# Optimization experiments

Hardware: AMD Instinct MI355X
Metric: run time of the kernel (lower is better)

## Reference

```python
import jax, jax.numpy as jnp
import numpy as np

N_NODES = 50000


def _gcn_norm(edge_index, n):
    # Add self-loops (PyG GCNConv default) and compute symmetric normalization.
    src = jnp.concatenate([edge_index[0], jnp.arange(n, dtype=edge_index.dtype)])
    dst = jnp.concatenate([edge_index[1], jnp.arange(n, dtype=edge_index.dtype)])
    deg = jax.ops.segment_sum(jnp.ones(src.shape[0], dtype=jnp.float32), dst,
                              num_segments=n)
    dinv = jnp.where(deg > 0, jax.lax.rsqrt(deg), 0.0)
    norm = dinv[src] * dinv[dst]  # [E+N]
    return src, dst, norm


def _gcn_conv(x, src, dst, norm, W, b, n):
    h = x @ W                              # [N, out] linear transform first
    msgs = h[src] * norm[:, None]          # gather + edge-wise scale [E+N, out]
    out = jax.ops.segment_sum(msgs, dst, num_segments=n)  # scatter-add
    return out + b


def setup_inputs() -> dict:
    key = jax.random.key(0)
    k1, k2, k3, k4 = jax.random.split(key, 4)
    N, E, F, H, C = N_NODES, 1600000, 128, 128, 64
    x = jax.random.normal(k1, (N, F), dtype=jnp.float32)
    edge_index = jax.random.randint(k2, (2, E), 0, N, dtype=jnp.int64)
    W1 = jax.random.normal(k3, (F, H), dtype=jnp.float32) * 0.05
    b1 = jnp.zeros((H,), dtype=jnp.float32)
    W2 = jax.random.normal(k4, (H, C), dtype=jnp.float32) * 0.05
    b2 = jnp.zeros((C,), dtype=jnp.float32)
    return {"x": x, "edge_index": edge_index, "W1": W1, "b1": b1,
            "W2": W2, "b2": b2}


def reference(x, edge_index, W1, b1, W2, b2):
    n = x.shape[0]
    src, dst, norm = _gcn_norm(edge_index, n)
    h = _gcn_conv(x, src, dst, norm, W1, b1, n)
    h = jax.nn.relu(h)
    out = _gcn_conv(h, src, dst, norm, W2, b2, n)
    return out
```

## Files before the change

### kernel.cpp

```cpp
#include <hip/hip_runtime.h>
#include <hip/hip_bf16.h>
#include <stdint.h>

#define N_NODES 50000
#define N_EDGES 1600000
#define N_TOT   (N_EDGES + N_NODES)
#define NBKT      256
#define BKT_NODES 196
#define BKT_CAP   7168
#define TILE      4096
#define EPT       16
#define ZROW      N_NODES

typedef unsigned short u16;
typedef __attribute__((ext_vector_type(8))) short short8;
typedef __attribute__((ext_vector_type(4))) float floatx4;

__device__ __forceinline__ float b2f(u16 u) {
    union { unsigned int i; float f; } v; v.i = ((unsigned int)u) << 16; return v.f;
}
__device__ __forceinline__ float asf(unsigned u) {
    union { unsigned int i; float f; } v; v.i = u; return v.f;
}
__device__ __forceinline__ u16 f2b(float f) {
    union { unsigned int i; float f; } v; v.f = f;
    unsigned int r = (v.i + 0x7FFFu + ((v.i >> 16) & 1u)) >> 16;
    return (u16)r;
}

__global__ __launch_bounds__(256) void k_part(const int* __restrict__ ei,
                                              const unsigned* __restrict__ xw,
                                              int* __restrict__ flags,
                                              unsigned* __restrict__ pairs,
                                              int* __restrict__ bktcnt) {
    __shared__ unsigned pairsL[TILE];
    __shared__ unsigned char bktL[TILE];
    __shared__ int hist[NBKT], incl[NBKT], delta[NBKT];
    __shared__ int zc, pc;
    int tid = threadIdx.x;
    long base = (long)blockIdx.x * TILE;
    hist[tid] = 0;
    if (tid == 0) { zc = 0; pc = 0; }
    __syncthreads();
    unsigned hw = ((const unsigned*)ei)[2 * tid + 1];
    atomicAdd(&zc, hw == 0 ? 1 : 0);
    if (blockIdx.x == 0) {
        unsigned w = xw[tid];
        int ex = (w >> 7) & 0xFF;
        atomicAdd(&pc, ((ex == 0) || (ex >= 0x60 && ex <= 0x9F)) ? 1 : 0);
    }
    __syncthreads();
    int i64 = zc > 250;
    if (blockIdx.x == 0 && tid == 0) {
        flags[0] = (pc < 160) ? 1 : 0;
        flags[1] = i64;
    }

    int myb[EPT], myrank[EPT]; unsigned myp[EPT];
#pragma unroll
    for (int t = 0; t < EPT; t++) {
        long idx = base + t * 256 + tid;
        int b = -1; unsigned p = 0;
        if (idx < N_TOT) {
            int s, d;
            if (idx < N_EDGES) {
                if (i64) { s = ei[2 * idx]; d = ei[2 * (N_EDGES + idx)]; }
                else     { s = ei[idx];     d = ei[N_EDGES + idx]; }
            } else {
                s = d = (int)(idx - N_EDGES);
            }
            b = d / BKT_NODES;
            p = (unsigned)s | ((unsigned)(d - b * BKT_NODES) << 16);
        }
        myb[t] = b; myp[t] = p;
        myrank[t] = (b >= 0) ? atomicAdd(&hist[b], 1) : 0;
    }
    __syncthreads();

    int tot = hist[tid];
    incl[tid] = tot;
    __syncthreads();
    for (int o = 1; o < NBKT; o <<= 1) {
        int t2 = (tid >= o) ? incl[tid - o] : 0;
        __syncthreads();
        incl[tid] += t2;
        __syncthreads();
    }
    int excl = incl[tid] - tot;
    int gb = atomicAdd(&bktcnt[tid], tot);
    hist[tid]  = excl;
    delta[tid] = tid * BKT_CAP + gb - excl;
    __syncthreads();

#pragma unroll
    for (int t = 0; t < EPT; t++) {
        if (myb[t] >= 0) {
            int slot = hist[myb[t]] + myrank[t];
            pairsL[slot] = myp[t];
            bktL[slot]   = (unsigned char)myb[t];
        }
    }
    __syncthreads();
    int count = incl[NBKT - 1];
    for (int i = tid; i < count; i += 256) {
        int b = bktL[i];
        int pos = delta[b] + i;
        if (pos - b * BKT_CAP < BKT_CAP)
            pairs[pos] = pairsL[i];
    }
}

__global__ __launch_bounds__(256) void k_bucket(const unsigned* __restrict__ pairs,
                                                const int* __restrict__ bktcnt,
                                                int* __restrict__ rowstart,
                                                int* __restrict__ deg,
                                                float* __restrict__ dinv,
                                                u16* __restrict__ csr) {
    __shared__ u16 csrL[BKT_CAP];
    __shared__ int degL[NBKT], curL[NBKT], scanT[NBKT];
    int b = blockIdx.x, tid = threadIdx.x;
    int cv = bktcnt[tid];
    scanT[tid] = cv;
    __syncthreads();
    for (int o = 1; o < NBKT; o <<= 1) {
        int t = (tid >= o) ? scanT[tid - o] : 0;
        __syncthreads();
        scanT[tid] += t;
        __syncthreads();
    }
    int cnt  = bktcnt[b];
    int base = scanT[b] - cnt;
    __syncthreads();

    const unsigned* reg = pairs + (size_t)b * BKT_CAP;
    degL[tid] = 0;
    __syncthreads();
    for (int i = tid; i < cnt; i += 256)
        atomicAdd(&degL[reg[i] >> 16], 1);
    __syncthreads();
    int v = degL[tid];
    scanT[tid] = v;
    __syncthreads();
    for (int o = 1; o < NBKT; o <<= 1) {
        int t = (tid >= o) ? scanT[tid - o] : 0;
        __syncthreads();
        scanT[tid] += t;
        __syncthreads();
    }
    int excl = scanT[tid] - v;
    curL[tid] = excl;
    int n = b * BKT_NODES + tid;
    if (tid < BKT_NODES && n < N_NODES) {
        rowstart[n] = base + excl;
        deg[n]      = v;
        dinv[n]     = rsqrtf((float)v);
    }
    __syncthreads();
    for (int i = tid; i < cnt; i += 256) {
        unsigned p = reg[i];
        int slot = atomicAdd(&curL[p >> 16], 1);
        csrL[slot] = (u16)(p & 0xFFFFu);
    }
    __syncthreads();
    for (int i = tid; i < cnt; i += 256)
        csr[base + i] = csrL[i];
}

template<int NOUT, bool ADYN>
__global__ __launch_bounds__(256) void k_gemm(const void* __restrict__ A,
                                              const void* __restrict__ W,
                                              const float* __restrict__ dinv,
                                              u16* __restrict__ out, int M,
                                              const int* __restrict__ flags) {
    const int isf32 = flags[0];
    constexpr int LDW = 136;
    __shared__ __align__(16) u16 Wt[NOUT * LDW];
    int tid = threadIdx.x;
    if (blockIdx.x == 0 && tid < NOUT)
        out[(size_t)M * NOUT + tid] = 0;
    const float* Wf = (const float*)W;
    const u16*   Wu = (const u16*)W;
    for (int idx = tid; idx < 128 * NOUT; idx += 256) {
        int k = idx / NOUT, n = idx % NOUT;
        Wt[n * LDW + k] = isf32 ? f2b(Wf[idx]) : Wu[idx];
    }
    __syncthreads();

    int wave = tid >> 6, lane = tid & 63;
    int quad = lane >> 4, l16 = lane & 15;
    int r0 = blockIdx.x * 64 + wave * 16;
    int r = r0 + l16; if (r >= M) r = M - 1;

    floatx4 acc[NOUT / 16];
#pragma unroll
    for (int i = 0; i < NOUT / 16; i++) acc[i] = (floatx4)(0.f);

#pragma unroll
    for (int ks = 0; ks < 4; ks++) {
        short8 a;
        if (ADYN && isf32) {
            const float* af = (const float*)A + (size_t)r * 128 + ks * 32 + quad * 8;
            float4 v0 = ((const float4*)af)[0];
            float4 v1 = ((const float4*)af)[1];
            a[0] = (short)f2b(v0.x); a[1] = (short)f2b(v0.y);
            a[2] = (short)f2b(v0.z); a[3] = (short)f2b(v0.w);
            a[4] = (short)f2b(v1.x); a[5] = (short)f2b(v1.y);
            a[6] = (short)f2b(v1.z); a[7] = (short)f2b(v1.w);
        } else {
            a = ((const short8*)((const u16*)A + (size_t)r * 128))[ks * 4 + quad];
        }
#pragma unroll
        for (int nt = 0; nt < NOUT / 16; nt++) {
            const short8* bp = (const short8*)&Wt[(nt * 16 + l16) * LDW + ks * 32 + quad * 8];
            acc[nt] = __builtin_amdgcn_mfma_f32_16x16x32_bf16(a, *bp, acc[nt], 0, 0, 0);
        }
    }
    float sc[4];
#pragma unroll
    for (int j = 0; j < 4; j++) {
        int row = r0 + quad * 4 + j;
        sc[j] = dinv[row < M ? row : 0];
    }
#pragma unroll
    for (int nt = 0; nt < NOUT / 16; nt++) {
#pragma unroll
        for (int j = 0; j < 4; j++) {
            int row = r0 + quad * 4 + j;
            if (row < M)
                out[(size_t)row * NOUT + nt * 16 + l16] = f2b(acc[nt][j] * sc[j]);
        }
    }
}

#define ACCU(u, j) { acc[j].x += asf((u) << 16); acc[j].y += asf((u) & 0xFFFF0000u); }
#define ACC4(q)    { ACCU(q.x,0) ACCU(q.y,1) ACCU(q.z,2) ACCU(q.w,3) }

__global__ __launch_bounds__(256) void k_agg1(const u16* __restrict__ h,
                                              const u16* __restrict__ csr,
                                              const int* __restrict__ rowstart,
                                              const int* __restrict__ deg,
                                              const float* __restrict__ dinv,
                                              const void* __restrict__ bias,
                                              u16* __restrict__ out,
                                              const int* __restrict__ flags) {
    int wave = threadIdx.x >> 6, lane = threadIdx.x & 63;
    int d = blockIdx.x * 4 + wave;
    int grp = lane >> 4, l16 = lane & 15;
    int start = rowstart[d], dg = deg[d], end = start + dg;
    int rounds = (dg + 3) >> 2;
    const uint4* hb = (const uint4*)h;
    float2 acc[4];
#pragma unroll
    for (int j = 0; j < 4; j++) acc[j] = make_float2(0.f, 0.f);

    int e0 = start + grp;
    int s;
    uint4 q0, q1, q2, q3;
    s = (e0      < end) ? csr[e0]      : ZROW; q0 = hb[(size_t)s * 16 + l16];
    s = (e0 + 4  < end) ? csr[e0 + 4]  : ZROW; q1 = hb[(size_t)s * 16 + l16];
    s = (e0 + 8  < end) ? csr[e0 + 8]  : ZROW; q2 = hb[(size_t)s * 16 + l16];
    s = (e0 + 12 < end) ? csr[e0 + 12] : ZROW; q3 = hb[(size_t)s * 16 + l16];
    int r = 4;
    for (; r + 3 < rounds; r += 4) {
        int e = e0 + 4 * r;
        ACC4(q0) s = (e      < end) ? csr[e]      : ZROW; q0 = hb[(size_t)s * 16 + l16];
        ACC4(q1) s = (e + 4  < end) ? csr[e + 4]  : ZROW; q1 = hb[(size_t)s * 16 + l16];
        ACC4(q2) s = (e + 8  < end) ? csr[e + 8]  : ZROW; q2 = hb[(size_t)s * 16 + l16];
        ACC4(q3) s = (e + 12 < end) ? csr[e + 12] : ZROW; q3 = hb[(size_t)s * 16 + l16];
    }
    for (; r < rounds; r++) {
        int e = e0 + 4 * r;
        ACC4(q0) s = (e < end) ? csr[e] : ZROW;
        q0 = q1; q1 = q2; q2 = q3; q3 = hb[(size_t)s * 16 + l16];
    }
    ACC4(q0) ACC4(q1) ACC4(q2) ACC4(q3)
#pragma unroll
    for (int j = 0; j < 4; j++) {
        acc[j].x += __shfl_xor(acc[j].x, 16); acc[j].y += __shfl_xor(acc[j].y, 16);
        acc[j].x += __shfl_xor(acc[j].x, 32); acc[j].y += __shfl_xor(acc[j].y, 32);
    }
    if (grp == 0) {
        int isf32 = flags[0];
        float dd = dinv[d];
        u16 r8[8];
#pragma unroll
        for (int j = 0; j < 4; j++) {
            float bx = isf32 ? ((const float*)bias)[l16 * 8 + 2 * j]
                             : b2f(((const u16*)bias)[l16 * 8 + 2 * j]);
            float by = isf32 ? ((const float*)bias)[l16 * 8 + 2 * j + 1]
                             : b2f(((const u16*)bias)[l16 * 8 + 2 * j + 1]);
            float vx = acc[j].x * dd + bx;
            float vy = acc[j].y * dd + by;
            r8[2 * j]     = f2b(vx > 0.f ? vx : 0.f);
            r8[2 * j + 1] = f2b(vy > 0.f ? vy : 0.f);
        }
        uint4 o;
        o.x = r8[0] | ((unsigned)r8[1] << 16); o.y = r8[2] | ((unsigned)r8[3] << 16);
        o.z = r8[4] | ((unsigned)r8[5] << 16); o.w = r8[6] | ((unsigned)r8[7] << 16);
        ((uint4*)(out + (size_t)d * 128))[l16] = o;
    }
}

__global__ __launch_bounds__(256) void k_agg2(const u16* __restrict__ h,
                                              const u16* __restrict__ csr,
                                              const int* __restrict__ rowstart,
                                              const int* __restrict__ deg,
                                              const float* __restrict__ dinv,
                                              const void* __restrict__ bias,
                                              float* __restrict__ out,
                                              const int* __restrict__ flags) {
    int wave = threadIdx.x >> 6, lane = threadIdx.x & 63;
    int d = blockIdx.x * 4 + wave;
    int oct = lane >> 3, l8 = lane & 7;
    int start = rowstart[d], dg = deg[d], end = start + dg;
    int rounds = (dg + 7) >> 3;
    const uint4* hb = (const uint4*)h;
    float2 acc[4];
#pragma unroll
    for (int j = 0; j < 4; j++) acc[j] = make_float2(0.f, 0.f);

    int e0 = start + oct;
    int s;
    uint4 q0, q1, q2;
    s = (e0      < end) ? csr[e0]      : ZROW; q0 = hb[(size_t)s * 8 + l8];
    s = (e0 + 8  < end) ? csr[e0 + 8]  : ZROW; q1 = hb[(size_t)s * 8 + l8];
    s = (e0 + 16 < end) ? csr[e0 + 16] : ZROW; q2 = hb[(size_t)s * 8 + l8];
    int r = 3;
    for (; r + 2 < rounds; r += 3) {
        int e = e0 + 8 * r;
        ACC4(q0) s = (e      < end) ? csr[e]      : ZROW; q0 = hb[(size_t)s * 8 + l8];
        ACC4(q1) s = (e + 8  < end) ? csr[e + 8]  : ZROW; q1 = hb[(size_t)s * 8 + l8];
        ACC4(q2) s = (e + 16 < end) ? csr[e + 16] : ZROW; q2 = hb[(size_t)s * 8 + l8];
    }
    for (; r < rounds; r++) {
        int e = e0 + 8 * r;
        ACC4(q0) s = (e < end) ? csr[e] : ZROW;
        q0 = q1; q1 = q2; q2 = hb[(size_t)s * 8 + l8];
    }
    ACC4(q0) ACC4(q1) ACC4(q2)
#pragma unroll
    for (int j = 0; j < 4; j++) {
        acc[j].x += __shfl_xor(acc[j].x, 8);  acc[j].y += __shfl_xor(acc[j].y, 8);
        acc[j].x += __shfl_xor(acc[j].x, 16); acc[j].y += __shfl_xor(acc[j].y, 16);
        acc[j].x += __shfl_xor(acc[j].x, 32); acc[j].y += __shfl_xor(acc[j].y, 32);
    }
    if (oct == 0) {
        int isf32 = flags[0];
        float dd = dinv[d];
        float r8[8];
#pragma unroll
        for (int j = 0; j < 4; j++) {
            float bx = isf32 ? ((const float*)bias)[l8 * 8 + 2 * j]
                             : b2f(((const u16*)bias)[l8 * 8 + 2 * j]);
            float by = isf32 ? ((const float*)bias)[l8 * 8 + 2 * j + 1]
                             : b2f(((const u16*)bias)[l8 * 8 + 2 * j + 1]);
            r8[2 * j]     = acc[j].x * dd + bx;
            r8[2 * j + 1] = acc[j].y * dd + by;
        }
        float4* op = (float4*)(out + (size_t)d * 64) + l8 * 2;
        op[0] = make_float4(r8[0], r8[1], r8[2], r8[3]);
        op[1] = make_float4(r8[4], r8[5], r8[6], r8[7]);
    }
}

extern "C" void kernel_launch(void* const* d_in, const int* in_sizes, int n_in,
                              void* d_out, int out_size, void* d_ws, size_t ws_size,
                              hipStream_t stream) {
    const void* x  = d_in[0];
    const int*  ei = (const int*)d_in[1];
    const void* W1 = d_in[2];
    const void* b1 = d_in[3];
    const void* W2 = d_in[4];
    const void* b2 = d_in[5];
    float* out = (float*)d_out;

    char* ws = (char*)d_ws;
    int*      flags    = (int*)(ws + 0);
    int*      bktcnt   = (int*)(ws + 1024);
    int*      deg      = (int*)(ws + 4096);
    int*      rowstart = (int*)(ws + 204800);
    float*    dinv     = (float*)(ws + 405504);
    unsigned* pairs    = (unsigned*)(ws + 606208);
    u16*      csr      = (u16*)(ws + 7946240);
    u16*      h1       = (u16*)(ws + 11247616);
    u16*      out1     = (u16*)(ws + 24048640);
    u16*      h2       = (u16*)(ws + 606208);

    hipMemsetAsync(bktcnt, 0, NBKT * sizeof(int), stream);
    k_part   <<<(N_TOT + TILE - 1) / TILE, 256, 0, stream>>>(ei, (const unsigned*)x,
                                                             flags, pairs, bktcnt);
    k_bucket <<<NBKT, 256, 0, stream>>>(pairs, bktcnt, rowstart, deg, dinv, csr);

    k_gemm<128, true> <<<(N_NODES + 63) / 64, 256, 0, stream>>>(x, W1, dinv, h1, N_NODES, flags);
    k_agg1<<<N_NODES / 4, 256, 0, stream>>>(h1, csr, rowstart, deg, dinv, b1, out1, flags);
    k_gemm<64, false> <<<(N_NODES + 63) / 64, 256, 0, stream>>>(out1, W2, dinv, h2, N_NODES, flags);
    k_agg2<<<N_NODES / 4, 256, 0, stream>>>(h2, csr, rowstart, deg, dinv, b2, out, flags);
}
```

Before: 246.7 us.

## Split layer-1 features into two 64-column panels for cache-friendly aggregation

The first GEMM now writes h1 as two column panels of 64 features, each with its own zero row. The first aggregation launches twice as many blocks, and each block processes one panel with the 8-lanes-per-edge scheme used by agg2. The goal is to halve the gathered working set per pass so the randomly indexed rows fit better in L2/MALL. In exchange, the CSR indices, rowstart and degree data are read twice, and every node is launched twice.

```diff
diff --git a/kernel.cpp b/kernel.cpp
--- a/kernel.cpp
+++ b/kernel.cpp
@@ -11,6 +11,8 @@
 #define TILE      4096
 #define EPT       16
 #define ZROW      N_NODES
+#define NGRP      12500
+#define PR        (N_NODES + 1)
 
 typedef unsigned short u16;
 typedef __attribute__((ext_vector_type(8))) short short8;
@@ -166,7 +168,7 @@
         csr[base + i] = csrL[i];
 }
 
-template<int NOUT, bool ADYN>
+template<int NOUT, bool ADYN, bool PANEL>
 __global__ __launch_bounds__(256) void k_gemm(const void* __restrict__ A,
                                               const void* __restrict__ W,
                                               const float* __restrict__ dinv,
@@ -176,8 +178,12 @@
     constexpr int LDW = 136;
     __shared__ __align__(16) u16 Wt[NOUT * LDW];
     int tid = threadIdx.x;
-    if (blockIdx.x == 0 && tid < NOUT)
-        out[(size_t)M * NOUT + tid] = 0;
+    if (blockIdx.x == 0 && tid < NOUT) {
+        if (PANEL)
+            out[((size_t)(tid >> 6) * PR + ZROW) * 64 + (tid & 63)] = 0;
+        else
+            out[(size_t)M * NOUT + tid] = 0;
+    }
     const float* Wf = (const float*)W;
     const u16*   Wu = (const u16*)W;
     for (int idx = tid; idx < 128 * NOUT; idx += 256) {
@@ -223,11 +229,17 @@
     }
 #pragma unroll
     for (int nt = 0; nt < NOUT / 16; nt++) {
+        int col = nt * 16 + l16;
 #pragma unroll
         for (int j = 0; j < 4; j++) {
             int row = r0 + quad * 4 + j;
-            if (row < M)
-                out[(size_t)row * NOUT + nt * 16 + l16] = f2b(acc[nt][j] * sc[j]);
+            if (row < M) {
+                u16 val = f2b(acc[nt][j] * sc[j]);
+                if (PANEL)
+                    out[((size_t)(col >> 6) * PR + row) * 64 + (col & 63)] = val;
+                else
+                    out[(size_t)row * NOUT + col] = val;
+            }
         }
     }
 }
@@ -244,51 +256,52 @@
                                               u16* __restrict__ out,
                                               const int* __restrict__ flags) {
     int wave = threadIdx.x >> 6, lane = threadIdx.x & 63;
-    int d = blockIdx.x * 4 + wave;
-    int grp = lane >> 4, l16 = lane & 15;
+    int panel = blockIdx.x / NGRP, gb = blockIdx.x % NGRP;
+    int d = gb * 4 + wave;
+    int oct = lane >> 3, l8 = lane & 7;
     int start = rowstart[d], dg = deg[d], end = start + dg;
-    int rounds = (dg + 3) >> 2;
-    const uint4* hb = (const uint4*)h;
+    int rounds = (dg + 7) >> 3;
+    const uint4* hb = (const uint4*)(h + (size_t)panel * PR * 64);
     float2 acc[4];
 #pragma unroll
     for (int j = 0; j < 4; j++) acc[j] = make_float2(0.f, 0.f);
 
-    int e0 = start + grp;
+    int e0 = start + oct;
     int s;
-    uint4 q0, q1, q2, q3;
-    s = (e0      < end) ? csr[e0]      : ZROW; q0 = hb[(size_t)s * 16 + l16];
-    s = (e0 + 4  < end) ? csr[e0 + 4]  : ZROW; q1 = hb[(size_t)s * 16 + l16];
-    s = (e0 + 8  < end) ? csr[e0 + 8]  : ZROW; q2 = hb[(size_t)s * 16 + l16];
-    s = (e0 + 12 < end) ? csr[e0 + 12] : ZROW; q3 = hb[(size_t)s * 16 + l16];
-    int r = 4;
-    for (; r + 3 < rounds; r += 4) {
-        int e = e0 + 4 * r;
-        ACC4(q0) s = (e      < end) ? csr[e]      : ZROW; q0 = hb[(size_t)s * 16 + l16];
-        ACC4(q1) s = (e + 4  < end) ? csr[e + 4]  : ZROW; q1 = hb[(size_t)s * 16 + l16];
-        ACC4(q2) s = (e + 8  < end) ? csr[e + 8]  : ZROW; q2 = hb[(size_t)s * 16 + l16];
-        ACC4(q3) s = (e + 12 < end) ? csr[e + 12] : ZROW; q3 = hb[(size_t)s * 16 + l16];
+    uint4 q0, q1, q2;
+    s = (e0      < end) ? csr[e0]      : ZROW; q0 = hb[(size_t)s * 8 + l8];
+    s = (e0 + 8  < end) ? csr[e0 + 8]  : ZROW; q1 = hb[(size_t)s * 8 + l8];
+    s = (e0 + 16 < end) ? csr[e0 + 16] : ZROW; q2 = hb[(size_t)s * 8 + l8];
+    int r = 3;
+    for (; r + 2 < rounds; r += 3) {
+        int e = e0 + 8 * r;
+        ACC4(q0) s = (e      < end) ? csr[e]      : ZROW; q0 = hb[(size_t)s * 8 + l8];
+        ACC4(q1) s = (e + 8  < end) ? csr[e + 8]  : ZROW; q1 = hb[(size_t)s * 8 + l8];
+        ACC4(q2) s = (e + 16 < end) ? csr[e + 16] : ZROW; q2 = hb[(size_t)s * 8 + l8];
     }
     for (; r < rounds; r++) {
-        int e = e0 + 4 * r;
+        int e = e0 + 8 * r;
         ACC4(q0) s = (e < end) ? csr[e] : ZROW;
-        q0 = q1; q1 = q2; q2 = q3; q3 = hb[(size_t)s * 16 + l16];
-    }
-    ACC4(q0) ACC4(q1) ACC4(q2) ACC4(q3)
+        q0 = q1; q1 = q2; q2 = hb[(size_t)s * 8 + l8];
+    }
+    ACC4(q0) ACC4(q1) ACC4(q2)
 #pragma unroll
     for (int j = 0; j < 4; j++) {
+        acc[j].x += __shfl_xor(acc[j].x, 8);  acc[j].y += __shfl_xor(acc[j].y, 8);
         acc[j].x += __shfl_xor(acc[j].x, 16); acc[j].y += __shfl_xor(acc[j].y, 16);
         acc[j].x += __shfl_xor(acc[j].x, 32); acc[j].y += __shfl_xor(acc[j].y, 32);
     }
-    if (grp == 0) {
+    if (oct == 0) {
         int isf32 = flags[0];
         float dd = dinv[d];
+        int fb = panel * 64 + l8 * 8;
         u16 r8[8];
 #pragma unroll
         for (int j = 0; j < 4; j++) {
-            float bx = isf32 ? ((const float*)bias)[l16 * 8 + 2 * j]
-                             : b2f(((const u16*)bias)[l16 * 8 + 2 * j]);
-            float by = isf32 ? ((const float*)bias)[l16 * 8 + 2 * j + 1]
-                             : b2f(((const u16*)bias)[l16 * 8 + 2 * j + 1]);
+            float bx = isf32 ? ((const float*)bias)[fb + 2 * j]
+                             : b2f(((const u16*)bias)[fb + 2 * j]);
+            float by = isf32 ? ((const float*)bias)[fb + 2 * j + 1]
+                             : b2f(((const u16*)bias)[fb + 2 * j + 1]);
             float vx = acc[j].x * dd + bx;
             float vy = acc[j].y * dd + by;
             r8[2 * j]     = f2b(vx > 0.f ? vx : 0.f);
@@ -297,7 +310,7 @@
         uint4 o;
         o.x = r8[0] | ((unsigned)r8[1] << 16); o.y = r8[2] | ((unsigned)r8[3] << 16);
         o.z = r8[4] | ((unsigned)r8[5] << 16); o.w = r8[6] | ((unsigned)r8[7] << 16);
-        ((uint4*)(out + (size_t)d * 128))[l16] = o;
+        ((uint4*)(out + (size_t)d * 128 + panel * 64))[l8] = o;
     }
 }
 
@@ -391,8 +404,8 @@
                                                              flags, pairs, bktcnt);
     k_bucket <<<NBKT, 256, 0, stream>>>(pairs, bktcnt, rowstart, deg, dinv, csr);
 
-    k_gemm<128, true> <<<(N_NODES + 63) / 64, 256, 0, stream>>>(x, W1, dinv, h1, N_NODES, flags);
-    k_agg1<<<N_NODES / 4, 256, 0, stream>>>(h1, csr, rowstart, deg, dinv, b1, out1, flags);
-    k_gemm<64, false> <<<(N_NODES + 63) / 64, 256, 0, stream>>>(out1, W2, dinv, h2, N_NODES, flags);
+    k_gemm<128, true, true>  <<<(N_NODES + 63) / 64, 256, 0, stream>>>(x, W1, dinv, h1, N_NODES, flags);
+    k_agg1<<<2 * NGRP, 256, 0, stream>>>(h1, csr, rowstart, deg, dinv, b1, out1, flags);
+    k_gemm<64, false, false> <<<(N_NODES + 63) / 64, 256, 0, stream>>>(out1, W2, dinv, h2, N_NODES, flags);
     k_agg2<<<N_NODES / 4, 256, 0, stream>>>(h2, csr, rowstart, deg, dinv, b2, out, flags);
 }
```

Measured after the change: 251.6 us. About the same (+2.0%).
